# Kernel tuning notes

Measured on AMD Instinct MI355X. Metric: run time of the kernel, lower is better.

## Reference

```python
import jax, jax.numpy as jnp
import numpy as np
from functools import partial

S, E, K = 50000, 20000, 128
B = 16384
NE = 1000000
L = 2  # num_layer


def setup_inputs() -> dict:
    key = jax.random.key(0)
    ks = jax.random.split(key, 24)
    inp = {
        'stu_id': jax.random.randint(ks[0], (B,), 0, S),
        'input_exercise': jax.random.randint(ks[1], (B,), 0, E),
        'input_knowledge_point': jax.random.uniform(ks[2], (B, K), jnp.float32),
        'rows_1': jax.random.randint(ks[3], (NE,), 0, S),
        'cols_1': jax.random.randint(ks[4], (NE,), 0, E),
        'rows_0': jax.random.randint(ks[5], (NE,), 0, S),
        'cols_0': jax.random.randint(ks[6], (NE,), 0, E),
        'vals_ui_1': jax.random.uniform(ks[7], (NE,), jnp.float32),
        'vals_iu_1': jax.random.uniform(ks[8], (NE,), jnp.float32),
        'vals_ui_0': jax.random.uniform(ks[9], (NE,), jnp.float32),
        'vals_iu_0': jax.random.uniform(ks[10], (NE,), jnp.float32),
        'd_i_1': jax.random.uniform(ks[11], (S,), jnp.float32),
        'd_j_1': jax.random.uniform(ks[12], (E,), jnp.float32),
        'd_i_0': jax.random.uniform(ks[13], (S,), jnp.float32),
        'd_j_0': jax.random.uniform(ks[14], (E,), jnp.float32),
        'student_emb': jax.random.normal(ks[15], (S, K), jnp.float32) * 0.1,
        'exercise_emb': jax.random.normal(ks[16], (E, K), jnp.float32) * 0.1,
        'student_emb_bias': jax.random.normal(ks[17], (S, 1), jnp.float32) * 0.1,
        'e_discrimination': jax.random.normal(ks[18], (E, 1), jnp.float32) * 0.1,
        'W1': jax.random.normal(ks[19], (256, K), jnp.float32) * (1.0 / np.sqrt(K)),
        'b1': jnp.zeros((256,), jnp.float32),
        'W2': jax.random.normal(ks[20], (128, 256), jnp.float32) * (1.0 / np.sqrt(256)),
        'b2': jnp.zeros((128,), jnp.float32),
        'W3': jax.random.normal(ks[21], (1, 128), jnp.float32) * (1.0 / np.sqrt(128)),
        'b3': jnp.zeros((1,), jnp.float32),
    }
    return inp


def pos_linear(x, W, b):
    # PosLinear: weight = 2*relu(-W) + W  (== |W|)
    Wp = 2.0 * jax.nn.relu(-W) + W
    return x @ Wp.T + b


def spmm(vals, rows, cols, x, n_out):
    # sparse.mm(A, x) where A has entries vals at (rows, cols); gather cols of x, scatter-add to rows
    return jax.ops.segment_sum(vals[:, None] * x[cols], rows, num_segments=n_out)


def graph_repr(student_emb, exercise_emb,
               rows_1, cols_1, vals_ui_1, vals_iu_1,
               rows_0, cols_0, vals_ui_0, vals_iu_0,
               d_i_1, d_j_1, d_i_0, d_j_0):
    stat = student_emb          # [S, K]
    kdiff = exercise_emb        # [E, K]
    for _ in range(L):
        u1 = spmm(vals_ui_1, rows_1, cols_1, kdiff, S) + stat * d_i_1[:, None]
        i1 = spmm(vals_iu_1, cols_1, rows_1, stat, E) + kdiff * d_j_1[:, None]
        u0 = spmm(vals_ui_0, rows_0, cols_0, kdiff, S) + stat * d_i_0[:, None]
        i0 = spmm(vals_iu_0, cols_0, rows_0, stat, E) + kdiff * d_j_0[:, None]
        stat = u1 + u0
        kdiff = i1 + i0
    return stat, kdiff


def reference(stu_id, input_exercise, input_knowledge_point,
              rows_1, cols_1, rows_0, cols_0,
              vals_ui_1, vals_iu_1, vals_ui_0, vals_iu_0,
              d_i_1, d_j_1, d_i_0, d_j_0,
              student_emb, exercise_emb, student_emb_bias, e_discrimination,
              W1, b1, W2, b2, W3, b3):
    stat, kdiff = graph_repr(student_emb, exercise_emb,
                             rows_1, cols_1, vals_ui_1, vals_iu_1,
                             rows_0, cols_0, vals_ui_0, vals_iu_0,
                             d_i_1, d_j_1, d_i_0, d_j_0)
    e_disc = jax.nn.sigmoid(e_discrimination[input_exercise])          # [B, 1]
    stat_b = jax.nn.sigmoid(stat[stu_id] + student_emb_bias[stu_id])   # [B, K]
    kd = jax.nn.sigmoid(kdiff[input_exercise])                         # [B, K]
    x = input_knowledge_point * (stat_b - kd) * e_disc
    x = jnp.tanh(pos_linear(x, W1, b1))   # dropout is identity in eval
    x = jnp.tanh(pos_linear(x, W2, b2))
    out = jax.nn.sigmoid(pos_linear(x, W3, b3))
    return out.reshape(-1)
```

## Files before the change

kernel.cpp:

```cpp
#include <hip/hip_runtime.h>
#include <hip/hip_fp16.h>

#define S_N 50000
#define E_N 20000
#define K_N 128
#define B_N 16384
#define NE_N 1000000

#define S_PER_XCD 6250
#define E_PER_XCD 2500

#define SCAP 96
#define ECAP 176

#define NBKT 512
#define S_SUB 196
#define E_SUB 79
#define BKCAP 8704
#define OVL_BKTS 257

#define BK_BLOCKS 245
#define CVT_BLOCKS 4375
#define MARK_BLOCKS 32

typedef short bf16x8 __attribute__((ext_vector_type(8)));
typedef float f32x4 __attribute__((ext_vector_type(4)));
typedef int i32x4 __attribute__((ext_vector_type(4)));
typedef float f32x4v __attribute__((ext_vector_type(4)));
typedef unsigned u32x4 __attribute__((ext_vector_type(4)));

__device__ __forceinline__ float sigmoidf_(float v) {
    return 1.0f / (1.0f + __expf(-v));
}
__device__ __forceinline__ float tanh_fast(float v) {
    float e = __expf(2.0f * v);
    return 1.0f - 2.0f / (e + 1.0f);
}
__device__ __forceinline__ unsigned short f2bf(float v) {
    unsigned u = __float_as_uint(v);
    u += 0x7fffu + ((u >> 16) & 1u);
    return (unsigned short)(u >> 16);
}
__device__ __forceinline__ void split_bf(float v, unsigned short& hi, unsigned short& lo) {
    unsigned u = __float_as_uint(v);
    hi = (unsigned short)(u >> 16);
    float fh = __uint_as_float(u & 0xffff0000u);
    lo = f2bf(v - fh);
}
__device__ __forceinline__ float2 h2f2(unsigned u) {
    __half2 h = *(const __half2*)&u;
    return __half22float2(h);
}
__device__ __forceinline__ void accum8(float* acc, uint4 h, float v) {
    float2 p0 = h2f2(h.x);
    float2 p1 = h2f2(h.y);
    float2 p2 = h2f2(h.z);
    float2 p3 = h2f2(h.w);
    acc[0] = fmaf(v, p0.x, acc[0]); acc[1] = fmaf(v, p0.y, acc[1]);
    acc[2] = fmaf(v, p1.x, acc[2]); acc[3] = fmaf(v, p1.y, acc[3]);
    acc[4] = fmaf(v, p2.x, acc[4]); acc[5] = fmaf(v, p2.y, acc[5]);
    acc[6] = fmaf(v, p3.x, acc[6]); acc[7] = fmaf(v, p3.y, acc[7]);
}
__device__ __forceinline__ unsigned f2h2u(float a, float b) {
    __half2 h = __floats2half2_rn(a, b);
    return *(const unsigned*)&h;
}

__device__ __forceinline__ unsigned long long* bslot(
    unsigned long long* ovl, unsigned long long* fr, int b) {
    return (b < OVL_BKTS) ? ovl + (size_t)b * BKCAP
                          : fr + (size_t)(b - OVL_BKTS) * BKCAP;
}

__global__ __launch_bounds__(1024) void build_init(
    const i32x4* __restrict__ r1, const i32x4* __restrict__ c1,
    const f32x4v* __restrict__ vui1, const f32x4v* __restrict__ viu1,
    const i32x4* __restrict__ r0, const i32x4* __restrict__ c0,
    const f32x4v* __restrict__ vui0, const f32x4v* __restrict__ viu0,
    unsigned long long* __restrict__ bOvl, unsigned long long* __restrict__ bFr,
    int* __restrict__ gcur,
    const float2* __restrict__ sE, const float2* __restrict__ eE,
    __half2* __restrict__ sH, __half2* __restrict__ eH,
    const int* __restrict__ sid, const int* __restrict__ eid,
    unsigned* __restrict__ maskS, unsigned* __restrict__ maskE) {
    const int tid = threadIdx.x;
    if ((int)blockIdx.x >= BK_BLOCKS) {
        int rel = blockIdx.x - BK_BLOCKS;
        if (rel < CVT_BLOCKS) {
            int i = rel * 1024 + tid;
            const int nS = S_N * 64;
            if (i < nS) {
                float2 v = sE[i];
                sH[i] = __floats2half2_rn(v.x, v.y);
            } else {
                int j = i - nS;
                if (j < E_N * 64) {
                    float2 v = eE[j];
                    eH[j] = __floats2half2_rn(v.x, v.y);
                }
            }
        } else {
            int i = (rel - CVT_BLOCKS) * 1024 + tid;
            if (i < B_N) {
                int v = sid[i];
                atomicOr(&maskS[v >> 5], 1u << (v & 31));
            } else if (i < 2 * B_N) {
                int v = eid[i - B_N];
                atomicOr(&maskE[v >> 5], 1u << (v & 31));
            }
        }
        return;
    }
    __shared__ int hist[NBKT];
    __shared__ int base[NBKT];
    for (int b = tid; b < NBKT; b += 1024) hist[b] = 0;
    __syncthreads();
    const int NV = NE_N / 4;
    i32x4 rv[2], cv[2]; f32x4v av[2], bv[2];
    int bkt[16], lr[16];
#pragma unroll
    for (int rep = 0; rep < 2; ++rep) {
        int i = blockIdx.x * 2048 + rep * 1024 + tid;
        bool valid = i < 2 * NV;
        if (valid) {
            if (i < NV) {
                rv[rep] = __builtin_nontemporal_load(r1 + i);
                cv[rep] = __builtin_nontemporal_load(c1 + i);
                av[rep] = __builtin_nontemporal_load(vui1 + i);
                bv[rep] = __builtin_nontemporal_load(viu1 + i);
            } else {
                int j = i - NV;
                rv[rep] = __builtin_nontemporal_load(r0 + j);
                cv[rep] = __builtin_nontemporal_load(c0 + j);
                av[rep] = __builtin_nontemporal_load(vui0 + j);
                bv[rep] = __builtin_nontemporal_load(viu0 + j);
            }
        }
#pragma unroll
        for (int k = 0; k < 4; ++k) {
            int u = rep * 8 + k * 2;
            if (valid) {
                int r = rv[rep][k], c = cv[rep][k];
                int xs = r / S_PER_XCD;
                int ss = (r - xs * S_PER_XCD) / S_SUB;
                int xe = c / E_PER_XCD;
                int se = (c - xe * E_PER_XCD) / E_SUB;
                bkt[u] = ss * 8 + xs;
                bkt[u + 1] = 256 + se * 8 + xe;
                lr[u] = atomicAdd(&hist[bkt[u]], 1);
                lr[u + 1] = atomicAdd(&hist[bkt[u + 1]], 1);
            } else {
                bkt[u] = -1; bkt[u + 1] = -1;
            }
        }
    }
    __syncthreads();
    for (int b = tid; b < NBKT; b += 1024) {
        int h = hist[b];
        base[b] = h ? atomicAdd(&gcur[b], h) : 0;
    }
    __syncthreads();
#pragma unroll
    for (int rep = 0; rep < 2; ++rep) {
#pragma unroll
        for (int k = 0; k < 4; ++k) {
            int u = rep * 8 + k * 2;
            if (bkt[u] >= 0) {
                int r = rv[rep][k], c = cv[rep][k];
                unsigned entS = ((unsigned)f2bf(av[rep][k]) << 16) | (unsigned)c;
                unsigned entE = ((unsigned)f2bf(bv[rep][k]) << 16) | (unsigned)r;
                int pS = base[bkt[u]] + lr[u];
                int pE = base[bkt[u + 1]] + lr[u + 1];
                if (pS < BKCAP)
                    bslot(bOvl, bFr, bkt[u])[pS] =
                        ((unsigned long long)(unsigned)r << 32) | entS;
                if (pE < BKCAP)
                    bslot(bOvl, bFr, bkt[u + 1])[pE] =
                        ((unsigned long long)(unsigned)c << 32) | entE;
            }
        }
    }
}

__global__ __launch_bounds__(1024) void scatter2(
    unsigned long long* __restrict__ bOvl, unsigned long long* __restrict__ bFr,
    const int* __restrict__ gcur,
    int* __restrict__ cntS, int* __restrict__ cntE,
    unsigned* __restrict__ csrS, unsigned* __restrict__ csrE) {
    __shared__ int lcnt[S_SUB];
    const int bid = blockIdx.x;
    const int tid = threadIdx.x;
    const bool isS = bid < 256;
    const int x = bid & 7;
    const int s = (isS ? bid : bid - 256) >> 3;
    const int start = isS ? x * S_PER_XCD + s * S_SUB : x * E_PER_XCD + s * E_SUB;
    const int len = isS ? min(S_SUB, S_PER_XCD - s * S_SUB)
                        : min(E_SUB, E_PER_XCD - s * E_SUB);
    for (int l = tid; l < len; l += 1024) lcnt[l] = 0;
    __syncthreads();
    int n = gcur[bid];
    if (n > BKCAP) n = BKCAP;
    const unsigned long long* bp = bslot(bOvl, bFr, bid);
    for (int i = tid; i < n; i += 1024) {
        unsigned long long v = __builtin_nontemporal_load(bp + i);
        int node = (int)(v >> 32);
        unsigned entry = (unsigned)v;
        int slot = atomicAdd(&lcnt[node - start], 1);
        if (isS) {
            if (slot < SCAP) csrS[(size_t)node * SCAP + slot] = entry;
        } else {
            if (slot < ECAP) csrE[(size_t)node * ECAP + slot] = entry;
        }
    }
    __syncthreads();
    for (int l = tid; l < len; l += 1024) {
        if (isS) cntS[start + l] = min(lcnt[l], SCAP);
        else     cntE[start + l] = min(lcnt[l], ECAP);
    }
}

__device__ __forceinline__ void gather_row(
    const uint4* __restrict__ src, const uint4* __restrict__ self,
    const float* __restrict__ dA, const float* __restrict__ dB,
    const int* __restrict__ cnt, const unsigned* __restrict__ csr,
    const unsigned* __restrict__ need,
    uint4* __restrict__ dst, int nrow, int cap, int w, int lane) {
    int slot = lane >> 4;
    int seg = lane & 15;
    if (w >= nrow) return;
    if (need && !((need[w >> 5] >> (w & 31)) & 1u)) return;
    int n = cnt[w];
    if (n > cap) n = cap;
    const unsigned* cbase = csr + (size_t)w * cap;
    float acc[8] = {};
    int i = 0;
    for (; i + 16 <= n; i += 16) {
        unsigned qa = __builtin_nontemporal_load(cbase + i + slot);
        unsigned qb = __builtin_nontemporal_load(cbase + i + 4 + slot);
        unsigned qc = __builtin_nontemporal_load(cbase + i + 8 + slot);
        unsigned qd = __builtin_nontemporal_load(cbase + i + 12 + slot);
        uint4 ha = src[(size_t)(qa & 0xffffu) * 16 + seg];
        uint4 hb = src[(size_t)(qb & 0xffffu) * 16 + seg];
        uint4 hc = src[(size_t)(qc & 0xffffu) * 16 + seg];
        uint4 hd = src[(size_t)(qd & 0xffffu) * 16 + seg];
        accum8(acc, ha, __uint_as_float(qa & 0xffff0000u));
        accum8(acc, hb, __uint_as_float(qb & 0xffff0000u));
        accum8(acc, hc, __uint_as_float(qc & 0xffff0000u));
        accum8(acc, hd, __uint_as_float(qd & 0xffff0000u));
    }
    for (; i + 8 <= n; i += 8) {
        unsigned qa = __builtin_nontemporal_load(cbase + i + slot);
        unsigned qb = __builtin_nontemporal_load(cbase + i + 4 + slot);
        uint4 ha = src[(size_t)(qa & 0xffffu) * 16 + seg];
        uint4 hb = src[(size_t)(qb & 0xffffu) * 16 + seg];
        accum8(acc, ha, __uint_as_float(qa & 0xffff0000u));
        accum8(acc, hb, __uint_as_float(qb & 0xffff0000u));
    }
    for (; i < n; i += 4) {
        int e = i + slot;
        if (e < n) {
            unsigned q = __builtin_nontemporal_load(cbase + e);
            uint4 h = src[(size_t)(q & 0xffffu) * 16 + seg];
            accum8(acc, h, __uint_as_float(q & 0xffff0000u));
        }
    }
#pragma unroll
    for (int j = 0; j < 8; ++j) {
        acc[j] += __shfl_xor(acc[j], 16);
        acc[j] += __shfl_xor(acc[j], 32);
    }
    if (slot == 0) {
        u32x4 hsv = __builtin_nontemporal_load(
            reinterpret_cast<const u32x4*>(self) + ((size_t)w * 16 + seg));
        unsigned h0 = hsv[0], h1 = hsv[1], h2 = hsv[2], h3 = hsv[3];
        float d = dA[w] + dB[w];
        float2 s0 = h2f2(h0);
        float2 s1 = h2f2(h1);
        float2 s2 = h2f2(h2);
        float2 s3 = h2f2(h3);
        u32x4 o;
        o[0] = f2h2u(fmaf(s0.x, d, acc[0]), fmaf(s0.y, d, acc[1]));
        o[1] = f2h2u(fmaf(s1.x, d, acc[2]), fmaf(s1.y, d, acc[3]));
        o[2] = f2h2u(fmaf(s2.x, d, acc[4]), fmaf(s2.y, d, acc[5]));
        o[3] = f2h2u(fmaf(s3.x, d, acc[6]), fmaf(s3.y, d, acc[7]));
        __builtin_nontemporal_store(
            o, reinterpret_cast<u32x4*>(dst) + ((size_t)w * 16 + seg));
    }
}

__global__ __launch_bounds__(256) void gather_dual(
    const uint4* __restrict__ srcE, const uint4* __restrict__ selfE,
    const float* __restrict__ dEA, const float* __restrict__ dEB,
    const int* __restrict__ cntEp, const unsigned* __restrict__ csrEp,
    const unsigned* __restrict__ needE, uint4* __restrict__ dstE,
    const uint4* __restrict__ srcS, const uint4* __restrict__ selfS,
    const float* __restrict__ dSA, const float* __restrict__ dSB,
    const int* __restrict__ cntSp, const unsigned* __restrict__ csrSp,
    const unsigned* __restrict__ needS, uint4* __restrict__ dstS,
    int eBlocks) {
    int lane = threadIdx.x & 63;
    int sub = threadIdx.x >> 6;
    if ((int)blockIdx.x < eBlocks) {
        int w = blockIdx.x * 4 + sub;
        gather_row(srcE, selfE, dEA, dEB, cntEp, csrEp, needE, dstE,
                   E_N, ECAP, w, lane);
    } else {
        int w = (blockIdx.x - eBlocks) * 4 + sub;
        gather_row(srcS, selfS, dSA, dSB, cntSp, csrSp, needS, dstS,
                   S_N, SCAP, w, lane);
    }
}

__global__ __launch_bounds__(256) void feature_abs_kernel(
    const int* __restrict__ stu_id, const int* __restrict__ ex_id,
    const float* __restrict__ ikp,
    const __half2* __restrict__ statH, const __half2* __restrict__ kdiffH,
    const float* __restrict__ s_bias, const float* __restrict__ e_disc,
    unsigned short* __restrict__ xhi, unsigned short* __restrict__ xlo,
    const float* __restrict__ W1, const float* __restrict__ W2,
    unsigned short* __restrict__ w1hi, unsigned short* __restrict__ w1lo,
    unsigned short* __restrict__ w2hi, unsigned short* __restrict__ w2lo,
    int featBlocks) {
    if ((int)blockIdx.x >= featBlocks) {
        int i = (blockIdx.x - featBlocks) * 256 + threadIdx.x;
        unsigned short hi, lo;
        if (i < 32768) {
            split_bf(fabsf(W1[i]), hi, lo);
            w1hi[i] = hi; w1lo[i] = lo;
        } else {
            int j = i - 32768;
            split_bf(fabsf(W2[j]), hi, lo);
            w2hi[j] = hi; w2lo[j] = lo;
        }
        return;
    }
    int i = blockIdx.x * 256 + threadIdx.x;
    int row = i >> 5;
    int k4 = (i & 31) * 4;
    int s = stu_id[row];
    int e = ex_id[row];
    float sb = s_bias[s];
    float ed = sigmoidf_(e_disc[e]);
    float2 s01 = __half22float2(statH[(size_t)s * 64 + (k4 >> 1)]);
    float2 s23 = __half22float2(statH[(size_t)s * 64 + (k4 >> 1) + 1]);
    float2 k01 = __half22float2(kdiffH[(size_t)e * 64 + (k4 >> 1)]);
    float2 k23 = __half22float2(kdiffH[(size_t)e * 64 + (k4 >> 1) + 1]);
    float4 iv = *(const float4*)(ikp + (size_t)row * K_N + k4);
    float f0 = iv.x * (sigmoidf_(s01.x + sb) - sigmoidf_(k01.x)) * ed;
    float f1 = iv.y * (sigmoidf_(s01.y + sb) - sigmoidf_(k01.y)) * ed;
    float f2 = iv.z * (sigmoidf_(s23.x + sb) - sigmoidf_(k23.x)) * ed;
    float f3 = iv.w * (sigmoidf_(s23.y + sb) - sigmoidf_(k23.y)) * ed;
    ushort4 oh, ol;
    split_bf(f0, oh.x, ol.x);
    split_bf(f1, oh.y, ol.y);
    split_bf(f2, oh.z, ol.z);
    split_bf(f3, oh.w, ol.w);
    *(ushort4*)(xhi + (size_t)row * K_N + k4) = oh;
    *(ushort4*)(xlo + (size_t)row * K_N + k4) = ol;
}

#define H1S 264

__global__ __launch_bounds__(256) void mlp_mfma(
    const unsigned short* __restrict__ xhi, const unsigned short* __restrict__ xlo,
    const unsigned short* __restrict__ w1hi, const unsigned short* __restrict__ w1lo,
    const unsigned short* __restrict__ w2hi, const unsigned short* __restrict__ w2lo,
    const float* __restrict__ b1, const float* __restrict__ b2,
    const float* __restrict__ W3, const float* __restrict__ b3,
    float* __restrict__ out) {
    __shared__ unsigned short h1hi[32 * H1S];
    __shared__ unsigned short h1lo[32 * H1S];
    __shared__ float partial[4][32];

    const int t = threadIdx.x;
    const int lane = t & 63;
    const int w = t >> 6;
    const int l15 = lane & 15;
    const int quad = lane >> 4;
    const int r0 = blockIdx.x * 32;

    f32x4 acc1[2][4] = {};
    for (int ks = 0; ks < 128; ks += 32) {
        bf16x8 ah[2], al[2], bh[4], bl[4];
#pragma unroll
        for (int mt = 0; mt < 2; ++mt) {
            size_t o = (size_t)(r0 + mt * 16 + l15) * K_N + ks + quad * 8;
            ah[mt] = *(const bf16x8*)(xhi + o);
            al[mt] = *(const bf16x8*)(xlo + o);
        }
#pragma unroll
        for (int nt = 0; nt < 4; ++nt) {
            size_t o = (size_t)(w * 64 + nt * 16 + l15) * 128 + ks + quad * 8;
            bh[nt] = *(const bf16x8*)(w1hi + o);
            bl[nt] = *(const bf16x8*)(w1lo + o);
        }
#pragma unroll
        for (int mt = 0; mt < 2; ++mt)
#pragma unroll
            for (int nt = 0; nt < 4; ++nt) {
                acc1[mt][nt] = __builtin_amdgcn_mfma_f32_16x16x32_bf16(
                    ah[mt], bh[nt], acc1[mt][nt], 0, 0, 0);
                acc1[mt][nt] = __builtin_amdgcn_mfma_f32_16x16x32_bf16(
                    ah[mt], bl[nt], acc1[mt][nt], 0, 0, 0);
                acc1[mt][nt] = __builtin_amdgcn_mfma_f32_16x16x32_bf16(
                    al[mt], bh[nt], acc1[mt][nt], 0, 0, 0);
            }
    }
#pragma unroll
    for (int nt = 0; nt < 4; ++nt) {
        int c = w * 64 + nt * 16 + l15;
        float bias = b1[c];
#pragma unroll
        for (int mt = 0; mt < 2; ++mt)
#pragma unroll
            for (int rg = 0; rg < 4; ++rg) {
                int row = mt * 16 + quad * 4 + rg;
                float h = tanh_fast(acc1[mt][nt][rg] + bias);
                unsigned short hi, lo;
                split_bf(h, hi, lo);
                h1hi[row * H1S + c] = hi;
                h1lo[row * H1S + c] = lo;
            }
    }
    __syncthreads();

    f32x4 acc2[2][2] = {};
    for (int ks = 0; ks < 256; ks += 32) {
        bf16x8 ah[2], al[2], bh[2], bl[2];
#pragma unroll
        for (int mt = 0; mt < 2; ++mt) {
            int o = (mt * 16 + l15) * H1S + ks + quad * 8;
            ah[mt] = *(const bf16x8*)(&h1hi[o]);
            al[mt] = *(const bf16x8*)(&h1lo[o]);
        }
#pragma unroll
        for (int nt = 0; nt < 2; ++nt) {
            size_t o = (size_t)(w * 32 + nt * 16 + l15) * 256 + ks + quad * 8;
            bh[nt] = *(const bf16x8*)(w2hi + o);
            bl[nt] = *(const bf16x8*)(w2lo + o);
        }
#pragma unroll
        for (int mt = 0; mt < 2; ++mt)
#pragma unroll
            for (int nt = 0; nt < 2; ++nt) {
                acc2[mt][nt] = __builtin_amdgcn_mfma_f32_16x16x32_bf16(
                    ah[mt], bh[nt], acc2[mt][nt], 0, 0, 0);
                acc2[mt][nt] = __builtin_amdgcn_mfma_f32_16x16x32_bf16(
                    ah[mt], bl[nt], acc2[mt][nt], 0, 0, 0);
                acc2[mt][nt] = __builtin_amdgcn_mfma_f32_16x16x32_bf16(
                    al[mt], bh[nt], acc2[mt][nt], 0, 0, 0);
            }
    }

    float w3v[2], b2v[2];
#pragma unroll
    for (int nt = 0; nt < 2; ++nt) {
        int c = w * 32 + nt * 16 + l15;
        w3v[nt] = fabsf(W3[c]);
        b2v[nt] = b2[c];
    }
#pragma unroll
    for (int mt = 0; mt < 2; ++mt)
#pragma unroll
        for (int rg = 0; rg < 4; ++rg) {
            float v = w3v[0] * tanh_fast(acc2[mt][0][rg] + b2v[0]) +
                      w3v[1] * tanh_fast(acc2[mt][1][rg] + b2v[1]);
            v += __shfl_xor(v, 1, 16);
            v += __shfl_xor(v, 2, 16);
            v += __shfl_xor(v, 4, 16);
            v += __shfl_xor(v, 8, 16);
            if (l15 == 0) partial[w][mt * 16 + quad * 4 + rg] = v;
        }
    __syncthreads();
    if (t < 32) {
        float v = partial[0][t] + partial[1][t] + partial[2][t] + partial[3][t];
        out[r0 + t] = sigmoidf_(v + b3[0]);
    }
}

extern "C" void kernel_launch(void* const* d_in, const int* in_sizes, int n_in,
                              void* d_out, int out_size, void* d_ws, size_t ws_size,
                              hipStream_t stream) {
    const int* stu_id        = (const int*)d_in[0];
    const int* input_ex      = (const int*)d_in[1];
    const float* ikp         = (const float*)d_in[2];
    const int* rows_1        = (const int*)d_in[3];
    const int* cols_1        = (const int*)d_in[4];
    const int* rows_0        = (const int*)d_in[5];
    const int* cols_0        = (const int*)d_in[6];
    const float* vals_ui_1   = (const float*)d_in[7];
    const float* vals_iu_1   = (const float*)d_in[8];
    const float* vals_ui_0   = (const float*)d_in[9];
    const float* vals_iu_0   = (const float*)d_in[10];
    const float* d_i_1       = (const float*)d_in[11];
    const float* d_j_1       = (const float*)d_in[12];
    const float* d_i_0       = (const float*)d_in[13];
    const float* d_j_0       = (const float*)d_in[14];
    const float* student_emb = (const float*)d_in[15];
    const float* exercise_emb= (const float*)d_in[16];
    const float* s_bias      = (const float*)d_in[17];
    const float* e_disc      = (const float*)d_in[18];
    const float* W1          = (const float*)d_in[19];
    const float* b1          = (const float*)d_in[20];
    const float* W2          = (const float*)d_in[21];
    const float* b2          = (const float*)d_in[22];
    const float* W3          = (const float*)d_in[23];
    const float* b3          = (const float*)d_in[24];

    char* p = (char*)d_ws;
    __half2* sEH     = (__half2*)p; p += (size_t)S_N * K_N * 2;
    __half2* eEH     = (__half2*)p; p += (size_t)E_N * K_N * 2;
    __half2* statAH  = (__half2*)p; p += (size_t)S_N * K_N * 2;
    __half2* kdiffAH = (__half2*)p; p += (size_t)E_N * K_N * 2;
    unsigned* csrS = (unsigned*)p; p += (size_t)S_N * SCAP * 4;
    unsigned* csrE = (unsigned*)p; p += (size_t)E_N * ECAP * 4;
    int* cntS     = (int*)p;   p += (size_t)S_N * 4;
    int* cntE     = (int*)p;   p += (size_t)E_N * 4;
    unsigned* maskS = (unsigned*)p; p += 2048 * 4;
    unsigned* maskE = (unsigned*)p; p += 1024 * 4;
    int* cur      = (int*)p;   p += NBKT * 4;
    p = (char*)(((size_t)p + 255) & ~(size_t)255);
    unsigned long long* buckFr = (unsigned long long*)p;
    p += (size_t)(NBKT - OVL_BKTS) * BKCAP * 8;
    unsigned long long* buckOvl = (unsigned long long*)statAH;
    __half2* statBH  = sEH;
    __half2* kdiffBH = eEH;
    unsigned short* xhi = (unsigned short*)statAH;
    unsigned short* xlo = xhi + (size_t)B_N * K_N;
    unsigned short* w1hi = (unsigned short*)kdiffAH;
    unsigned short* w1lo = w1hi + 32768;
    unsigned short* w2hi = w1lo + 32768;
    unsigned short* w2lo = w2hi + 32768;

    hipMemsetAsync(maskS, 0, (2048 + 1024 + NBKT) * 4, stream);

    build_init<<<BK_BLOCKS + CVT_BLOCKS + MARK_BLOCKS, 1024, 0, stream>>>(
        (const i32x4*)rows_1, (const i32x4*)cols_1,
        (const f32x4v*)vals_ui_1, (const f32x4v*)vals_iu_1,
        (const i32x4*)rows_0, (const i32x4*)cols_0,
        (const f32x4v*)vals_ui_0, (const f32x4v*)vals_iu_0,
        buckOvl, buckFr, cur,
        (const float2*)student_emb, (const float2*)exercise_emb, sEH, eEH,
        stu_id, input_ex, maskS, maskE);

    scatter2<<<NBKT, 1024, 0, stream>>>(
        buckOvl, buckFr, cur, cntS, cntE, csrS, csrE);

    const int sGrid = (S_N + 3) / 4;
    const int eGrid = (E_N + 3) / 4;

    gather_dual<<<eGrid + sGrid, 256, 0, stream>>>(
        (const uint4*)sEH, (const uint4*)eEH, d_j_1, d_j_0,
        cntE, csrE, nullptr, (uint4*)kdiffAH,
        (const uint4*)eEH, (const uint4*)sEH, d_i_1, d_i_0,
        cntS, csrS, nullptr, (uint4*)statAH, eGrid);

    gather_dual<<<eGrid + sGrid, 256, 0, stream>>>(
        (const uint4*)statAH, (const uint4*)kdiffAH, d_j_1, d_j_0,
        cntE, csrE, maskE, (uint4*)kdiffBH,
        (const uint4*)kdiffAH, (const uint4*)statAH, d_i_1, d_i_0,
        cntS, csrS, maskS, (uint4*)statBH, eGrid);

    const int featBlocks = B_N * 32 / 256;
    feature_abs_kernel<<<featBlocks + 256, 256, 0, stream>>>(
        stu_id, input_ex, ikp, statBH, kdiffBH, s_bias, e_disc, xhi, xlo,
        W1, W2, w1hi, w1lo, w2hi, w2lo, featBlocks);
    mlp_mfma<<<B_N / 32, 256, 0, stream>>>(xhi, xlo, w1hi, w1lo, w2hi, w2lo,
                                           b1, b2, W3, b3, (float*)d_out);
}
```

Measured before the change: 380.4 us.

## Compact needed rows into lists for second-layer gather, move weight split earlier

scatter2 now builds compacted lists of the student and exercise rows that the batch actually references, using ballots and atomics. The second-layer gather launches over those lists instead of every row, so it no longer runs blocks whose warps only test a mask bit and exit. The |W| bf16 hi/lo split moves from the feature kernel into build_init, using new workspace buffers. The cost is extra atomics and list writes in scatter2 and an indirect row lookup in the gather, and list order breaks the locality of the row access pattern.

Result: no change. 380.9 us (+0.1%).

```diff
diff --git a/kernel.cpp b/kernel.cpp
--- a/kernel.cpp
+++ b/kernel.cpp
@@ -22,6 +22,7 @@
 #define BK_BLOCKS 245
 #define CVT_BLOCKS 4375
 #define MARK_BLOCKS 32
+#define W_BLOCKS 64
 
 typedef short bf16x8 __attribute__((ext_vector_type(8)));
 typedef float f32x4 __attribute__((ext_vector_type(4)));
@@ -82,7 +83,10 @@
     const float2* __restrict__ sE, const float2* __restrict__ eE,
     __half2* __restrict__ sH, __half2* __restrict__ eH,
     const int* __restrict__ sid, const int* __restrict__ eid,
-    unsigned* __restrict__ maskS, unsigned* __restrict__ maskE) {
+    unsigned* __restrict__ maskS, unsigned* __restrict__ maskE,
+    const float* __restrict__ W1, const float* __restrict__ W2,
+    unsigned short* __restrict__ w1hi, unsigned short* __restrict__ w1lo,
+    unsigned short* __restrict__ w2hi, unsigned short* __restrict__ w2lo) {
     const int tid = threadIdx.x;
     if ((int)blockIdx.x >= BK_BLOCKS) {
         int rel = blockIdx.x - BK_BLOCKS;
@@ -99,7 +103,7 @@
                     eH[j] = __floats2half2_rn(v.x, v.y);
                 }
             }
-        } else {
+        } else if (rel < CVT_BLOCKS + MARK_BLOCKS) {
             int i = (rel - CVT_BLOCKS) * 1024 + tid;
             if (i < B_N) {
                 int v = sid[i];
@@ -107,6 +111,17 @@
             } else if (i < 2 * B_N) {
                 int v = eid[i - B_N];
                 atomicOr(&maskE[v >> 5], 1u << (v & 31));
+            }
+        } else {
+            int i = (rel - CVT_BLOCKS - MARK_BLOCKS) * 1024 + tid;
+            unsigned short hi, lo;
+            if (i < 32768) {
+                split_bf(fabsf(W1[i]), hi, lo);
+                w1hi[i] = hi; w1lo[i] = lo;
+            } else {
+                int j = i - 32768;
+                split_bf(fabsf(W2[j]), hi, lo);
+                w2hi[j] = hi; w2lo[j] = lo;
             }
         }
         return;
@@ -186,8 +201,14 @@
     unsigned long long* __restrict__ bOvl, unsigned long long* __restrict__ bFr,
     const int* __restrict__ gcur,
     int* __restrict__ cntS, int* __restrict__ cntE,
-    unsigned* __restrict__ csrS, unsigned* __restrict__ csrE) {
+    unsigned* __restrict__ csrS, unsigned* __restrict__ csrE,
+    const unsigned* __restrict__ maskS, const unsigned* __restrict__ maskE,
+    int* __restrict__ listS, int* __restrict__ listE,
+    int* __restrict__ lcntS, int* __restrict__ lcntE) {
     __shared__ int lcnt[S_SUB];
+    __shared__ int nlist[S_SUB];
+    __shared__ int blkCnt;
+    __shared__ int gBase;
     const int bid = blockIdx.x;
     const int tid = threadIdx.x;
     const bool isS = bid < 256;
@@ -197,6 +218,7 @@
     const int len = isS ? min(S_SUB, S_PER_XCD - s * S_SUB)
                         : min(E_SUB, E_PER_XCD - s * E_SUB);
     for (int l = tid; l < len; l += 1024) lcnt[l] = 0;
+    if (tid == 0) blkCnt = 0;
     __syncthreads();
     int n = gcur[bid];
     if (n > BKCAP) n = BKCAP;
@@ -213,24 +235,38 @@
         }
     }
     __syncthreads();
-    for (int l = tid; l < len; l += 1024) {
-        if (isS) cntS[start + l] = min(lcnt[l], SCAP);
-        else     cntE[start + l] = min(lcnt[l], ECAP);
-    }
-}
-
-__device__ __forceinline__ void gather_row(
+    const unsigned* mask = isS ? maskS : maskE;
+    bool needed = false;
+    int node = start + tid;
+    if (tid < len) {
+        int c = min(lcnt[tid], isS ? SCAP : ECAP);
+        if (isS) cntS[node] = c;
+        else     cntE[node] = c;
+        needed = (mask[node >> 5] >> (node & 31)) & 1u;
+    }
+    unsigned long long bal = __ballot(needed);
+    int lane = tid & 63;
+    int rank = __popcll(bal & ((1ull << lane) - 1));
+    int wcnt = __popcll(bal);
+    int wbase = 0;
+    if (lane == 0 && wcnt) wbase = atomicAdd(&blkCnt, wcnt);
+    wbase = __builtin_amdgcn_readfirstlane(wbase);
+    if (needed) nlist[wbase + rank] = node;
+    __syncthreads();
+    if (tid == 0 && blkCnt)
+        gBase = atomicAdd(isS ? lcntS : lcntE, blkCnt);
+    __syncthreads();
+    int* glist = isS ? listS : listE;
+    for (int l = tid; l < blkCnt; l += 1024) glist[gBase + l] = nlist[l];
+}
+
+__device__ __forceinline__ void gather_row_n(
     const uint4* __restrict__ src, const uint4* __restrict__ self,
     const float* __restrict__ dA, const float* __restrict__ dB,
-    const int* __restrict__ cnt, const unsigned* __restrict__ csr,
-    const unsigned* __restrict__ need,
-    uint4* __restrict__ dst, int nrow, int cap, int w, int lane) {
+    const unsigned* __restrict__ csr,
+    uint4* __restrict__ dst, int cap, int w, int lane, int n) {
     int slot = lane >> 4;
     int seg = lane & 15;
-    if (w >= nrow) return;
-    if (need && !((need[w >> 5] >> (w & 31)) & 1u)) return;
-    int n = cnt[w];
-    if (n > cap) n = cap;
     const unsigned* cbase = csr + (size_t)w * cap;
     float acc[8] = {};
     int i = 0;
@@ -292,48 +328,62 @@
     const uint4* __restrict__ srcE, const uint4* __restrict__ selfE,
     const float* __restrict__ dEA, const float* __restrict__ dEB,
     const int* __restrict__ cntEp, const unsigned* __restrict__ csrEp,
-    const unsigned* __restrict__ needE, uint4* __restrict__ dstE,
+    uint4* __restrict__ dstE,
     const uint4* __restrict__ srcS, const uint4* __restrict__ selfS,
     const float* __restrict__ dSA, const float* __restrict__ dSB,
     const int* __restrict__ cntSp, const unsigned* __restrict__ csrSp,
-    const unsigned* __restrict__ needS, uint4* __restrict__ dstS,
+    uint4* __restrict__ dstS,
     int eBlocks) {
     int lane = threadIdx.x & 63;
     int sub = threadIdx.x >> 6;
     if ((int)blockIdx.x < eBlocks) {
         int w = blockIdx.x * 4 + sub;
-        gather_row(srcE, selfE, dEA, dEB, cntEp, csrEp, needE, dstE,
-                   E_N, ECAP, w, lane);
+        if (w >= E_N) return;
+        int n = min(cntEp[w], ECAP);
+        gather_row_n(srcE, selfE, dEA, dEB, csrEp, dstE, ECAP, w, lane, n);
     } else {
         int w = (blockIdx.x - eBlocks) * 4 + sub;
-        gather_row(srcS, selfS, dSA, dSB, cntSp, csrSp, needS, dstS,
-                   S_N, SCAP, w, lane);
-    }
-}
-
-__global__ __launch_bounds__(256) void feature_abs_kernel(
+        if (w >= S_N) return;
+        int n = min(cntSp[w], SCAP);
+        gather_row_n(srcS, selfS, dSA, dSB, csrSp, dstS, SCAP, w, lane, n);
+    }
+}
+
+__global__ __launch_bounds__(256) void gather_list(
+    const uint4* __restrict__ srcE, const uint4* __restrict__ selfE,
+    const float* __restrict__ dEA, const float* __restrict__ dEB,
+    const int* __restrict__ cntEp, const unsigned* __restrict__ csrEp,
+    uint4* __restrict__ dstE,
+    const int* __restrict__ listE, const int* __restrict__ lcntE,
+    const uint4* __restrict__ srcS, const uint4* __restrict__ selfS,
+    const float* __restrict__ dSA, const float* __restrict__ dSB,
+    const int* __restrict__ cntSp, const unsigned* __restrict__ csrSp,
+    uint4* __restrict__ dstS,
+    const int* __restrict__ listS, const int* __restrict__ lcntS,
+    int eBlocks) {
+    int lane = threadIdx.x & 63;
+    int sub = threadIdx.x >> 6;
+    if ((int)blockIdx.x < eBlocks) {
+        int idx = blockIdx.x * 4 + sub;
+        if (idx >= *lcntE) return;
+        int w = listE[idx];
+        int n = min(cntEp[w], ECAP);
+        gather_row_n(srcE, selfE, dEA, dEB, csrEp, dstE, ECAP, w, lane, n);
+    } else {
+        int idx = (blockIdx.x - eBlocks) * 4 + sub;
+        if (idx >= *lcntS) return;
+        int w = listS[idx];
+        int n = min(cntSp[w], SCAP);
+        gather_row_n(srcS, selfS, dSA, dSB, csrSp, dstS, SCAP, w, lane, n);
+    }
+}
+
+__global__ __launch_bounds__(256) void feature_kernel(
     const int* __restrict__ stu_id, const int* __restrict__ ex_id,
     const float* __restrict__ ikp,
     const __half2* __restrict__ statH, const __half2* __restrict__ kdiffH,
     const float* __restrict__ s_bias, const float* __restrict__ e_disc,
-    unsigned short* __restrict__ xhi, unsigned short* __restrict__ xlo,
-    const float* __restrict__ W1, const float* __restrict__ W2,
-    unsigned short* __restrict__ w1hi, unsigned short* __restrict__ w1lo,
-    unsigned short* __restrict__ w2hi, unsigned short* __restrict__ w2lo,
-    int featBlocks) {
-    if ((int)blockIdx.x >= featBlocks) {
-        int i = (blockIdx.x - featBlocks) * 256 + threadIdx.x;
-        unsigned short hi, lo;
-        if (i < 32768) {
-            split_bf(fabsf(W1[i]), hi, lo);
-            w1hi[i] = hi; w1lo[i] = lo;
-        } else {
-            int j = i - 32768;
-            split_bf(fabsf(W2[j]), hi, lo);
-            w2hi[j] = hi; w2lo[j] = lo;
-        }
-        return;
-    }
+    unsigned short* __restrict__ xhi, unsigned short* __restrict__ xlo) {
     int i = blockIdx.x * 256 + threadIdx.x;
     int row = i >> 5;
     int k4 = (i & 31) * 4;
@@ -518,53 +568,59 @@
     int* cntE     = (int*)p;   p += (size_t)E_N * 4;
     unsigned* maskS = (unsigned*)p; p += 2048 * 4;
     unsigned* maskE = (unsigned*)p; p += 1024 * 4;
-    int* cur      = (int*)p;   p += NBKT * 4;
+    int* cur      = (int*)p;   p += (NBKT + 2) * 4;
     p = (char*)(((size_t)p + 255) & ~(size_t)255);
     unsigned long long* buckFr = (unsigned long long*)p;
     p += (size_t)(NBKT - OVL_BKTS) * BKCAP * 8;
+    unsigned short* w1hi = (unsigned short*)p; p += 32768 * 2;
+    unsigned short* w1lo = (unsigned short*)p; p += 32768 * 2;
+    unsigned short* w2hi = (unsigned short*)p; p += 32768 * 2;
+    unsigned short* w2lo = (unsigned short*)p; p += 32768 * 2;
+    int* listS = (int*)p; p += (size_t)B_N * 4;
+    int* listE = (int*)p; p += (size_t)B_N * 4;
     unsigned long long* buckOvl = (unsigned long long*)statAH;
+    int* lcntS = cur + NBKT;
+    int* lcntE = cur + NBKT + 1;
     __half2* statBH  = sEH;
     __half2* kdiffBH = eEH;
     unsigned short* xhi = (unsigned short*)statAH;
     unsigned short* xlo = xhi + (size_t)B_N * K_N;
-    unsigned short* w1hi = (unsigned short*)kdiffAH;
-    unsigned short* w1lo = w1hi + 32768;
-    unsigned short* w2hi = w1lo + 32768;
-    unsigned short* w2lo = w2hi + 32768;
-
-    hipMemsetAsync(maskS, 0, (2048 + 1024 + NBKT) * 4, stream);
-
-    build_init<<<BK_BLOCKS + CVT_BLOCKS + MARK_BLOCKS, 1024, 0, stream>>>(
+
+    hipMemsetAsync(maskS, 0, (2048 + 1024 + NBKT + 2) * 4, stream);
+
+    build_init<<<BK_BLOCKS + CVT_BLOCKS + MARK_BLOCKS + W_BLOCKS, 1024, 0, stream>>>(
         (const i32x4*)rows_1, (const i32x4*)cols_1,
         (const f32x4v*)vals_ui_1, (const f32x4v*)vals_iu_1,
         (const i32x4*)rows_0, (const i32x4*)cols_0,
         (const f32x4v*)vals_ui_0, (const f32x4v*)vals_iu_0,
         buckOvl, buckFr, cur,
         (const float2*)student_emb, (const float2*)exercise_emb, sEH, eEH,
-        stu_id, input_ex, maskS, maskE);
+        stu_id, input_ex, maskS, maskE,
+        W1, W2, w1hi, w1lo, w2hi, w2lo);
 
     scatter2<<<NBKT, 1024, 0, stream>>>(
-        buckOvl, buckFr, cur, cntS, cntE, csrS, csrE);
+        buckOvl, buckFr, cur, cntS, cntE, csrS, csrE,
+        maskS, maskE, listS, listE, lcntS, lcntE);
 
     const int sGrid = (S_N + 3) / 4;
     const int eGrid = (E_N + 3) / 4;
 
     gather_dual<<<eGrid + sGrid, 256, 0, stream>>>(
         (const uint4*)sEH, (const uint4*)eEH, d_j_1, d_j_0,
-        cntE, csrE, nullptr, (uint4*)kdiffAH,
+        cntE, csrE, (uint4*)kdiffAH,
         (const uint4*)eEH, (const uint4*)sEH, d_i_1, d_i_0,
-        cntS, csrS, nullptr, (uint4*)statAH, eGrid);
-
-    gather_dual<<<eGrid + sGrid, 256, 0, stream>>>(
+        cntS, csrS, (uint4*)statAH, eGrid);
+
+    const int eLBlk = (B_N + 3) / 4;
+    const int sLBlk = (B_N + 3) / 4;
+    gather_list<<<eLBlk + sLBlk, 256, 0, stream>>>(
         (const uint4*)statAH, (const uint4*)kdiffAH, d_j_1, d_j_0,
-        cntE, csrE, maskE, (uint4*)kdiffBH,
+        cntE, csrE, (uint4*)kdiffBH, listE, lcntE,
         (const uint4*)kdiffAH, (const uint4*)statAH, d_i_1, d_i_0,
-        cntS, csrS, maskS, (uint4*)statBH, eGrid);
-
-    const int featBlocks = B_N * 32 / 256;
-    feature_abs_kernel<<<featBlocks + 256, 256, 0, stream>>>(
-        stu_id, input_ex, ikp, statBH, kdiffBH, s_bias, e_disc, xhi, xlo,
-        W1, W2, w1hi, w1lo, w2hi, w2lo, featBlocks);
+        cntS, csrS, (uint4*)statBH, listS, lcntS, eLBlk);
+
+    feature_kernel<<<B_N * 32 / 256, 256, 0, stream>>>(
+        stu_id, input_ex, ikp, statBH, kdiffBH, s_bias, e_disc, xhi, xlo);
     mlp_mfma<<<B_N / 32, 256, 0, stream>>>(xhi, xlo, w1hi, w1lo, w2hi, w2lo,
                                            b1, b2, W3, b3, (float*)d_out);
 }
```
